# Kernel optimization log

Hardware: AMD Instinct MI355X
Metric: run time of the kernel (lower is better)

Reference implementation:

```python
import jax, jax.numpy as jnp
import numpy as np

B, T, NIN = 128, 256, 16
H1 = H2 = 512
NACT = 4
SLOPE = 25.0  # snntorch FastSigmoid default slope

@jax.custom_vjp
def spike(x):
    return (x > 0).astype(x.dtype)

def _spike_fwd(x):
    return (x > 0).astype(x.dtype), x

def _spike_bwd(x, g):
    # FastSigmoid surrogate: d/dx = 1 / (slope*|x| + 1)^2
    return (g / (SLOPE * jnp.abs(x) + 1.0) ** 2,)

spike.defvjp(_spike_fwd, _spike_bwd)

def setup_inputs() -> dict:
    key = jax.random.key(0)
    ks = jax.random.split(key, 12)
    def lin(k, fan_in, shape):
        lim = 1.0 / np.sqrt(fan_in)
        return jax.random.uniform(k, shape, jnp.float32, -lim, lim)
    return {
        "batch": jax.random.uniform(ks[0], (B, T, NIN), jnp.float32, 0.0, 2.5),
        "W1": lin(ks[1], NIN, (H1, NIN)), "b1": lin(ks[2], NIN, (H1,)),
        "beta1": jax.random.uniform(ks[3], (H1,), jnp.float32),
        "thr1": jax.random.uniform(ks[4], (H1,), jnp.float32),
        "W2": lin(ks[5], H1, (H2, H1)), "b2": lin(ks[6], H1, (H2,)),
        "beta2": jax.random.uniform(ks[7], (H2,), jnp.float32),
        "thr2": jax.random.uniform(ks[8], (H2,), jnp.float32),
        "Wa": lin(ks[9], H2, (NACT, H2)), "ba": lin(ks[10], H2, (NACT,)),
        "beta_act": jnp.float32(0.95),
        "inp_min": jnp.float32(0.0),
        "inp_max": jnp.float32(2.5),
    }

def _lif_subtract(cur, mem, beta, thr):
    # snntorch Leaky: reset from PRE-update membrane, detached; subtract reset
    reset = jax.lax.stop_gradient((mem - thr > 0).astype(mem.dtype))
    mem = jnp.clip(beta, 0.0, 1.0) * mem + cur - reset * thr
    return spike(mem - thr), mem

def reference(batch, W1, b1, beta1, thr1, W2, b2, beta2, thr2, Wa, ba, beta_act, inp_min, inp_max):
    Bb = batch.shape[0]
    x_seq = jnp.swapaxes(batch, 0, 1)  # [T, B, NIN]
    mem1 = jnp.zeros((Bb, W1.shape[0]), batch.dtype)
    mem2 = jnp.zeros((Bb, W2.shape[0]), batch.dtype)
    mem_a = jnp.zeros((Bb, Wa.shape[0]), batch.dtype)

    def step(carry, x):
        mem1, mem2, mem_a = carry
        x = (x - inp_min) / (inp_max - inp_min)
        spk1, mem1 = _lif_subtract(x @ W1.T + b1, mem1, beta1, thr1)
        spk2, mem2 = _lif_subtract(spk1 @ W2.T + b2, mem2, beta2, thr2)
        act = spk2 @ Wa.T + ba
        # action_lif: reset_mechanism='none', beta=0.95 learnable
        mem_a = jnp.clip(beta_act, 0.0, 1.0) * mem_a + act
        return (mem1, mem2, mem_a), mem_a.reshape(-1)  # torch: mem_act.reshape((1,-1))

    _, vals = jax.lax.scan(step, (mem1, mem2, mem_a), x_seq)
    # torch.stack(values, dim=1) of (1, B*NACT) tensors -> (1, T, B*NACT)
    return vals[None, :, :]
```

## Files before the change

### kernel.cpp

```cpp
#include <hip/hip_runtime.h>
#include <stdint.h>

typedef __attribute__((ext_vector_type(8))) short short8;
typedef __attribute__((ext_vector_type(4))) float f32x4;

#define T_STEPS 256
#define BATCH   128

#define LDS_BARRIER() asm volatile("s_waitcnt lgkmcnt(0)\n\ts_barrier" ::: "memory")

static __device__ inline unsigned short f2bf(float f) {
    unsigned int u = __float_as_uint(f);
    unsigned int r = u + 0x7FFFu + ((u >> 16) & 1u);
    return (unsigned short)(r >> 16);
}
static __device__ inline unsigned pack_hi16(unsigned a, unsigned b) {
    return (a >> 16) | (b & 0xFFFF0000u);
}

__global__ __launch_bounds__(256) void k_prep(
    const float* __restrict__ W2, const float* __restrict__ W1,
    const float* __restrict__ b1, const float* __restrict__ thr1,
    const float* __restrict__ imin_p, const float* __restrict__ imax_p,
    const float* __restrict__ batch,
    unsigned short* __restrict__ W2hi, unsigned short* __restrict__ W2lo,
    unsigned short* __restrict__ W1rows, float* __restrict__ b1s,
    unsigned short* __restrict__ Xf)
{
    int blk = blockIdx.x, tid = threadIdx.x;
    if (blk < 256) {
        int gid = blk * 256 + tid;
        f32x4 wv = *(const f32x4*)(W2 + (size_t)gid * 4);
        unsigned short hi[4], lo[4];
#pragma unroll
        for (int e = 0; e < 4; ++e) {
            float wf = wv[e];
            unsigned short h = f2bf(wf);
            float hf = __uint_as_float(((unsigned int)h) << 16);
            hi[e] = h;
            lo[e] = f2bf(wf - hf);
        }
        uint2 ph, pl;
        ph.x = (unsigned)hi[0] | ((unsigned)hi[1] << 16);
        ph.y = (unsigned)hi[2] | ((unsigned)hi[3] << 16);
        pl.x = (unsigned)lo[0] | ((unsigned)lo[1] << 16);
        pl.y = (unsigned)lo[2] | ((unsigned)lo[3] << 16);
        *(uint2*)(W2hi + (size_t)gid * 4) = ph;
        *(uint2*)(W2lo + (size_t)gid * 4) = pl;
    } else if (blk < 258) {
        int h = (blk - 256) * 256 + tid;
        float wsc = 1.0f / thr1[h];
        unsigned short row[64];
#pragma unroll
        for (int k = 0; k < 16; ++k) {
            float wv = W1[h * 16 + k] * wsc;
            unsigned a = __float_as_uint(wv) & 0xFFFF0000u;
            float r1 = wv - __uint_as_float(a);
            unsigned m = __float_as_uint(r1) & 0xFFFF0000u;
            float r2 = r1 - __uint_as_float(m);
            unsigned l = __float_as_uint(r2) & 0xFFFF0000u;
            row[k]      = (unsigned short)(a >> 16);
            row[16 + k] = (unsigned short)(m >> 16);
            row[32 + k] = (unsigned short)(l >> 16);
            row[48 + k] = 0;
        }
        b1s[h] = b1[h] * wsc;
        uint4* dst = (uint4*)(W1rows + (size_t)h * 64);
#pragma unroll
        for (int i = 0; i < 8; ++i) dst[i] = ((uint4*)row)[i];
    } else {
        int gid   = (blk - 258) * 256 + tid;
        int lane  = gid & 63;
        int btile = (gid >> 6) & 7;
        int t     = gid >> 9;
        int q     = lane >> 4, m15 = lane & 15;
        int b     = btile * 16 + m15;
        float imin = imin_p[0];
        float isc  = 1.0f / (imax_p[0] - imin);
        const float* xp = batch + ((size_t)b * T_STEPS + t) * 16 + (q & 1) * 8;
        unsigned uh[8], um[8], ul[8];
#pragma unroll
        for (int j = 0; j < 8; ++j) {
            float xv = (xp[j] - imin) * isc;
            unsigned a = __float_as_uint(xv) & 0xFFFF0000u;
            float r1 = xv - __uint_as_float(a);
            unsigned m = __float_as_uint(r1) & 0xFFFF0000u;
            float r2 = r1 - __uint_as_float(m);
            unsigned l = __float_as_uint(r2) & 0xFFFF0000u;
            uh[j] = a; um[j] = m; ul[j] = l;
        }
        uint4 B1, B2, XL;
        B1.x = pack_hi16(uh[0], uh[1]); B1.y = pack_hi16(uh[2], uh[3]);
        B1.z = pack_hi16(uh[4], uh[5]); B1.w = pack_hi16(uh[6], uh[7]);
        B2.x = pack_hi16(um[0], um[1]); B2.y = pack_hi16(um[2], um[3]);
        B2.z = pack_hi16(um[4], um[5]); B2.w = pack_hi16(um[6], um[7]);
        XL.x = pack_hi16(ul[0], ul[1]); XL.y = pack_hi16(ul[2], ul[3]);
        XL.z = pack_hi16(ul[4], ul[5]); XL.w = pack_hi16(ul[6], ul[7]);
        uint4 B3 = (q < 2) ? XL : B1;
        unsigned short* dst = Xf + (((size_t)t * 8 + btile) * 3) * 512 + lane * 8;
        *(uint4*)(dst +    0) = B1;
        *(uint4*)(dst +  512) = B2;
        *(uint4*)(dst + 1024) = B3;
    }
}

__global__ __launch_bounds__(1024, 4) void k_main(
    const unsigned short* __restrict__ Xf,
    const unsigned short* __restrict__ W2hi, const unsigned short* __restrict__ W2lo,
    const unsigned short* __restrict__ W1rows, const float* __restrict__ b1s,
    const float* __restrict__ beta1, const float* __restrict__ b2,
    const float* __restrict__ beta2, const float* __restrict__ thr2,
    unsigned short* __restrict__ spkbits)
{
    __shared__ unsigned short Aw[8192];
    __shared__ float Cbuf[2][4352];

    int tid  = threadIdx.x;
    int lane = tid & 63;
    int w    = tid >> 6;
    int q    = lane >> 4, m15 = lane & 15;
    int btile = blockIdx.x & 7;
    int slice = blockIdx.x >> 3;

    short8 A1[2], A2[2];
#pragma unroll
    for (int c = 0; c < 2; ++c) {
        const unsigned short* rp = W1rows + (size_t)(w * 32 + c * 16 + m15) * 64;
        A1[c] = *(const short8*)(rp + q * 8);
        A2[c] = *(const short8*)(rp + q * 8 + (q >> 1) * 16);
    }
    int jg = slice * 16 + m15;
    short8 bhi = *(const short8*)(W2hi + (size_t)jg * 512 + w * 32 + q * 8);
    short8 blo = *(const short8*)(W2lo + (size_t)jg * 512 + w * 32 + q * 8);

    f32x4 b14[2], bet1[2];
#pragma unroll
    for (int c = 0; c < 2; ++c) {
        int h0 = w * 32 + c * 16 + q * 4;
        b14[c] = *(const f32x4*)(b1s + h0);
        f32x4 bb = *(const f32x4*)(beta1 + h0);
#pragma unroll
        for (int r = 0; r < 4; ++r) bet1[c][r] = fminf(fmaxf(bb[r], 0.0f), 1.0f);
    }
    float m1[8], spk1f[8];
#pragma unroll
    for (int i = 0; i < 8; ++i) { m1[i] = 0.0f; spk1f[i] = 0.0f; }

    float beta2r = fminf(fmaxf(beta2[jg], 0.0f), 1.0f);
    float thr2r  = thr2[jg];
    float nthr2  = -thr2r;
    float b2r    = b2[jg];
    float m2 = 0.0f, spk2f = 0.0f;

    const unsigned short* xbase = Xf + ((size_t)btile * 3) * 512 + lane * 8;
    uint4 xc[3], xn[3];
#pragma unroll
    for (int f = 0; f < 3; ++f) xc[f] = *(const uint4*)(xbase + f * 512);

    unsigned short* myAw = Aw + w * 512;
    int wr0 = (0 * 2 + (q >> 1)) * 128 + (m15 ^ (q >> 1)) * 8 + (q & 1) * 4;
    int wr1 = (1 * 2 + (q >> 1)) * 128 + (m15 ^ (q >> 1)) * 8 + (q & 1) * 4;
    int rdo = (q * 16 + (m15 ^ (q & 1))) * 8;
    int p4  = (lane >> 4) * 4;

    auto body = [&](int ts, uint4* xcur, uint4* xnx) __attribute__((always_inline)) {
        int buf = ts & 1;
        int tn = (ts + 1 < T_STEPS) ? ts + 1 : ts;
        const unsigned short* xp = xbase + (size_t)tn * 12288;
#pragma unroll
        for (int f = 0; f < 3; ++f) xnx[f] = *(const uint4*)(xp + f * 512);

        union { uint4 u; short8 s; } Bf[3];
#pragma unroll
        for (int f = 0; f < 3; ++f) Bf[f].u = xcur[f];
        f32x4 D[2];
#pragma unroll
        for (int c = 0; c < 2; ++c) {
            D[c] = b14[c];
            D[c] = __builtin_amdgcn_mfma_f32_16x16x32_bf16(A1[c], Bf[0].s, D[c], 0, 0, 0);
            D[c] = __builtin_amdgcn_mfma_f32_16x16x32_bf16(A1[c], Bf[1].s, D[c], 0, 0, 0);
            D[c] = __builtin_amdgcn_mfma_f32_16x16x32_bf16(A2[c], Bf[2].s, D[c], 0, 0, 0);
        }
#pragma unroll
        for (int i = 0; i < 8; ++i) {
            int c = i >> 2, r = i & 3;
            float mv = fmaf(bet1[c][r], m1[i], D[c][r]);
            mv -= spk1f[i];
            bool sp = mv > 1.0f;
            m1[i] = mv;
            spk1f[i] = sp ? 1.0f : 0.0f;
        }
        {
            uint2 pk0, pk1;
            pk0.x = pack_hi16(__float_as_uint(spk1f[0]), __float_as_uint(spk1f[1]));
            pk0.y = pack_hi16(__float_as_uint(spk1f[2]), __float_as_uint(spk1f[3]));
            pk1.x = pack_hi16(__float_as_uint(spk1f[4]), __float_as_uint(spk1f[5]));
            pk1.y = pack_hi16(__float_as_uint(spk1f[6]), __float_as_uint(spk1f[7]));
            *(uint2*)(myAw + wr0) = pk0;
            *(uint2*)(myAw + wr1) = pk1;
        }
        union { uint4 u; short8 s; } af;
        af.u = *(uint4*)(myAw + rdo);
        f32x4 C2 = { 0.f, 0.f, 0.f, 0.f };
        C2 = __builtin_amdgcn_mfma_f32_16x16x32_bf16(af.s, bhi, C2, 0, 0, 0);
        C2 = __builtin_amdgcn_mfma_f32_16x16x32_bf16(af.s, blo, C2, 0, 0, 0);
#pragma unroll
        for (int r = 0; r < 4; ++r)
            Cbuf[buf][(q * 4 + r) * 272 + m15 * 17 + w] = C2[r];
        LDS_BARRIER();
        {
            float s0, s1, s2, s3;
            int base = w * 272 + m15 * 17 + p4;
            s0 = Cbuf[buf][base + 0];
            s1 = Cbuf[buf][base + 1];
            s2 = Cbuf[buf][base + 2];
            s3 = Cbuf[buf][base + 3];
            float s = (s0 + s1) + (s2 + s3);
            s += __shfl_xor(s, 16, 64);
            s += __shfl_xor(s, 32, 64);
            float cur2 = b2r + s;
            m2 = fmaf(beta2r, m2, cur2);
            m2 = fmaf(spk2f, nthr2, m2);
            bool sp2 = m2 > thr2r;
            spk2f = sp2 ? 1.0f : 0.0f;
            unsigned long long mask = __ballot(sp2);
            if (lane == 0) {
                spkbits[((size_t)ts * BATCH + btile * 16 + w) * 32 + slice] =
                    (unsigned short)(mask & 0xFFFFu);
            }
        }
    };

#pragma unroll 1
    for (int ts = 0; ts < T_STEPS; ts += 2) {
        body(ts, xc, xn);
        body(ts + 1, xn, xc);
    }
}

__global__ __launch_bounds__(256) void k_act(
    const unsigned short* __restrict__ spkbits,
    const float* __restrict__ Wa, const float* __restrict__ ba,
    const float* __restrict__ beta_act_p, float* __restrict__ out)
{
    __shared__ f32x4 waT[512];
    __shared__ f32x4 sc[256];
    int tid = threadIdx.x;
    int b   = blockIdx.x;

    for (int j = tid; j < 512; j += 256) {
        f32x4 v = { Wa[j], Wa[512 + j], Wa[1024 + j], Wa[1536 + j] };
        waT[j] = v;
    }
    float bact = fminf(fmaxf(beta_act_p[0], 0.0f), 1.0f);
    f32x4 acc = { ba[0], ba[1], ba[2], ba[3] };
    __syncthreads();

    const unsigned short* sp = spkbits + ((size_t)tid * BATCH + b) * 32;
    unsigned int wbuf[16];
#pragma unroll
    for (int r = 0; r < 4; ++r) {
        uint4 v = *(const uint4*)(sp + r * 8);
        wbuf[r*4+0] = v.x; wbuf[r*4+1] = v.y; wbuf[r*4+2] = v.z; wbuf[r*4+3] = v.w;
    }
    for (int s = 0; s < 32; ++s) {
        unsigned int wd = (wbuf[s >> 1] >> ((s & 1) * 16)) & 0xFFFFu;
#pragma unroll
        for (int i = 0; i < 16; ++i) {
            float sel = ((wd >> i) & 1u) ? 1.0f : 0.0f;
            f32x4 wv = waT[s * 16 + i];
            acc[0] = fmaf(sel, wv[0], acc[0]);
            acc[1] = fmaf(sel, wv[1], acc[1]);
            acc[2] = fmaf(sel, wv[2], acc[2]);
            acc[3] = fmaf(sel, wv[3], acc[3]);
        }
    }
    sc[tid] = acc;
    __syncthreads();
    float bd = bact;
    for (int d = 1; d < 256; d <<= 1) {
        f32x4 cv = sc[tid];
        f32x4 pv = { 0.f, 0.f, 0.f, 0.f };
        if (tid >= d) pv = sc[tid - d];
        __syncthreads();
        cv[0] = fmaf(bd, pv[0], cv[0]);
        cv[1] = fmaf(bd, pv[1], cv[1]);
        cv[2] = fmaf(bd, pv[2], cv[2]);
        cv[3] = fmaf(bd, pv[3], cv[3]);
        sc[tid] = cv;
        __syncthreads();
        bd *= bd;
    }
    f32x4 res = sc[tid];
    *(f32x4*)(out + (size_t)tid * 512 + b * 4) = res;
}

extern "C" void kernel_launch(void* const* d_in, const int* in_sizes, int n_in,
                              void* d_out, int out_size, void* d_ws, size_t ws_size,
                              hipStream_t stream)
{
    const float* batch    = (const float*)d_in[0];
    const float* W1       = (const float*)d_in[1];
    const float* b1       = (const float*)d_in[2];
    const float* beta1    = (const float*)d_in[3];
    const float* thr1     = (const float*)d_in[4];
    const float* W2       = (const float*)d_in[5];
    const float* b2       = (const float*)d_in[6];
    const float* beta2    = (const float*)d_in[7];
    const float* thr2     = (const float*)d_in[8];
    const float* Wa       = (const float*)d_in[9];
    const float* ba       = (const float*)d_in[10];
    const float* beta_act = (const float*)d_in[11];
    const float* inp_min  = (const float*)d_in[12];
    const float* inp_max  = (const float*)d_in[13];
    float* out            = (float*)d_out;

    char* ws = (char*)d_ws;
    unsigned short* W2hi    = (unsigned short*)ws;
    unsigned short* W2lo    = (unsigned short*)(ws + (512u << 10));
    unsigned short* W1rows  = (unsigned short*)(ws + (1u << 20));
    float*          b1s     = (float*)(ws + (1u << 20) + (64u << 10));
    unsigned short* Xf      = (unsigned short*)(ws + (2u << 20));
    unsigned short* spkbits = (unsigned short*)(ws + (8u << 20));

    hipLaunchKernelGGL(k_prep, dim3(770), dim3(256), 0, stream,
                       W2, W1, b1, thr1, inp_min, inp_max, batch,
                       W2hi, W2lo, W1rows, b1s, Xf);
    hipLaunchKernelGGL(k_main, dim3(256), dim3(1024), 0, stream,
                       Xf, W2hi, W2lo, W1rows, b1s, beta1, b2, beta2, thr2, spkbits);
    hipLaunchKernelGGL(k_act, dim3(128), dim3(256), 0, stream, spkbits, Wa, ba, beta_act, out);
}
```

Measured before the change: 313.4 us.

## Software-pipeline layer-1 compute with a two-stage LDS reduction of layer-2 partials

Restructures the main time loop so layer-1 MFMA work for step k+1 is issued before the cross-wave reduction of step k's layer-2 partial sums. The reduction is split into two LDS stages (Cbuf, then Sbuf) with a lane-contiguous layout, replacing the strided padded read and the shuffle-based reduction. Each wave now owns a subset of rows for the final LIF update. The aim is to hide the reduction latency behind the next step's compute, at the cost of an extra barrier per step and more LDS traffic.

```diff
diff --git a/kernel.cpp b/kernel.cpp
--- a/kernel.cpp
+++ b/kernel.cpp
@@ -113,7 +113,8 @@
     unsigned short* __restrict__ spkbits)
 {
     __shared__ unsigned short Aw[8192];
-    __shared__ float Cbuf[2][4352];
+    __shared__ float Cbuf[2][4096];
+    __shared__ float Sbuf[1024];
 
     int tid  = threadIdx.x;
     int lane = tid & 63;
@@ -121,6 +122,7 @@
     int q    = lane >> 4, m15 = lane & 15;
     int btile = blockIdx.x & 7;
     int slice = blockIdx.x >> 3;
+    int rr   = w & 3, gg = w >> 2;
 
     short8 A1[2], A2[2];
 #pragma unroll
@@ -153,19 +155,17 @@
     float m2 = 0.0f, spk2f = 0.0f;
 
     const unsigned short* xbase = Xf + ((size_t)btile * 3) * 512 + lane * 8;
-    uint4 xc[3], xn[3];
-#pragma unroll
-    for (int f = 0; f < 3; ++f) xc[f] = *(const uint4*)(xbase + f * 512);
+    uint4 xA[3], xB[3];
+#pragma unroll
+    for (int f = 0; f < 3; ++f) xA[f] = *(const uint4*)(xbase + f * 512);
 
     unsigned short* myAw = Aw + w * 512;
     int wr0 = (0 * 2 + (q >> 1)) * 128 + (m15 ^ (q >> 1)) * 8 + (q & 1) * 4;
     int wr1 = (1 * 2 + (q >> 1)) * 128 + (m15 ^ (q >> 1)) * 8 + (q & 1) * 4;
     int rdo = (q * 16 + (m15 ^ (q & 1))) * 8;
-    int p4  = (lane >> 4) * 4;
-
-    auto body = [&](int ts, uint4* xcur, uint4* xnx) __attribute__((always_inline)) {
-        int buf = ts & 1;
-        int tn = (ts + 1 < T_STEPS) ? ts + 1 : ts;
+
+    auto W = [&](int k, uint4* xcur, uint4* xnx) __attribute__((always_inline)) {
+        int tn = (k + 1 < T_STEPS) ? k + 1 : k;
         const unsigned short* xp = xbase + (size_t)tn * 12288;
 #pragma unroll
         for (int f = 0; f < 3; ++f) xnx[f] = *(const uint4*)(xp + f * 512);
@@ -204,37 +204,50 @@
         f32x4 C2 = { 0.f, 0.f, 0.f, 0.f };
         C2 = __builtin_amdgcn_mfma_f32_16x16x32_bf16(af.s, bhi, C2, 0, 0, 0);
         C2 = __builtin_amdgcn_mfma_f32_16x16x32_bf16(af.s, blo, C2, 0, 0, 0);
+        float* cb = Cbuf[k & 1];
 #pragma unroll
         for (int r = 0; r < 4; ++r)
-            Cbuf[buf][(q * 4 + r) * 272 + m15 * 17 + w] = C2[r];
+            cb[r * 1024 + w * 64 + lane] = C2[r];
+    };
+    auto S1 = [&](int i) __attribute__((always_inline)) {
+        const float* cb = Cbuf[i & 1];
+        float s0 = cb[rr * 1024 + (gg * 4 + 0) * 64 + lane];
+        float s1 = cb[rr * 1024 + (gg * 4 + 1) * 64 + lane];
+        float s2 = cb[rr * 1024 + (gg * 4 + 2) * 64 + lane];
+        float s3 = cb[rr * 1024 + (gg * 4 + 3) * 64 + lane];
+        Sbuf[(rr * 4 + gg) * 64 + lane] = (s0 + s1) + (s2 + s3);
+    };
+    auto S2 = [&](int i) __attribute__((always_inline)) {
+        float s0 = Sbuf[(rr * 4 + 0) * 64 + lane];
+        float s1 = Sbuf[(rr * 4 + 1) * 64 + lane];
+        float s2 = Sbuf[(rr * 4 + 2) * 64 + lane];
+        float s3 = Sbuf[(rr * 4 + 3) * 64 + lane];
+        float cur2 = b2r + ((s0 + s1) + (s2 + s3));
+        m2 = fmaf(beta2r, m2, cur2);
+        m2 = fmaf(spk2f, nthr2, m2);
+        bool sp2 = m2 > thr2r;
+        spk2f = sp2 ? 1.0f : 0.0f;
+        unsigned long long mask = __ballot(sp2);
+        if (w < 4 && m15 == 0) {
+            int p = lane >> 4;
+            spkbits[((size_t)i * BATCH + btile * 16 + p * 4 + w) * 32 + slice] =
+                (unsigned short)(mask >> (p * 16));
+        }
+    };
+
+    W(0, xA, xB);
+#pragma unroll 1
+    for (int i = 0; i < T_STEPS; i += 2) {
         LDS_BARRIER();
-        {
-            float s0, s1, s2, s3;
-            int base = w * 272 + m15 * 17 + p4;
-            s0 = Cbuf[buf][base + 0];
-            s1 = Cbuf[buf][base + 1];
-            s2 = Cbuf[buf][base + 2];
-            s3 = Cbuf[buf][base + 3];
-            float s = (s0 + s1) + (s2 + s3);
-            s += __shfl_xor(s, 16, 64);
-            s += __shfl_xor(s, 32, 64);
-            float cur2 = b2r + s;
-            m2 = fmaf(beta2r, m2, cur2);
-            m2 = fmaf(spk2f, nthr2, m2);
-            bool sp2 = m2 > thr2r;
-            spk2f = sp2 ? 1.0f : 0.0f;
-            unsigned long long mask = __ballot(sp2);
-            if (lane == 0) {
-                spkbits[((size_t)ts * BATCH + btile * 16 + w) * 32 + slice] =
-                    (unsigned short)(mask & 0xFFFFu);
-            }
-        }
-    };
-
-#pragma unroll 1
-    for (int ts = 0; ts < T_STEPS; ts += 2) {
-        body(ts, xc, xn);
-        body(ts + 1, xn, xc);
+        W(i + 1, xB, xA);
+        S1(i);
+        LDS_BARRIER();
+        S2(i);
+        LDS_BARRIER();
+        if (i + 2 < T_STEPS) W(i + 2, xA, xB);
+        S1(i + 1);
+        LDS_BARRIER();
+        S2(i + 1);
     }
 }
 
```

Result: slower. 332.5 us (+6.1%).

## Software-pipeline layer-2 reduction across timesteps with swizzled Cbuf layout

Applied to the files above, without the earlier changes.

Restructures the main time loop so each step's layer-2 reduction and spike emission run after the next step's layer-1 MFMA and LIF work. This lets the LDS reads overlap with compute, and the loop now needs only one barrier per step. The input prefetch distance is increased to two steps, and Cbuf switches from a padded stride-17 layout to an XOR-swizzled layout, which makes it smaller. The cost is extra register pressure from the deeper pipeline and a trickier prologue and epilogue, with a risk of off-by-one timing errors.

```diff
diff --git a/kernel.cpp b/kernel.cpp
--- a/kernel.cpp
+++ b/kernel.cpp
@@ -113,7 +113,7 @@
     unsigned short* __restrict__ spkbits)
 {
     __shared__ unsigned short Aw[8192];
-    __shared__ float Cbuf[2][4352];
+    __shared__ float Cbuf[2][4096];
 
     int tid  = threadIdx.x;
     int lane = tid & 63;
@@ -121,6 +121,7 @@
     int q    = lane >> 4, m15 = lane & 15;
     int btile = blockIdx.x & 7;
     int slice = blockIdx.x >> 3;
+    int rr = w & 3, qi = w >> 2;
 
     short8 A1[2], A2[2];
 #pragma unroll
@@ -153,34 +154,35 @@
     float m2 = 0.0f, spk2f = 0.0f;
 
     const unsigned short* xbase = Xf + ((size_t)btile * 3) * 512 + lane * 8;
-    uint4 xc[3], xn[3];
-#pragma unroll
-    for (int f = 0; f < 3; ++f) xc[f] = *(const uint4*)(xbase + f * 512);
-
-    unsigned short* myAw = Aw + w * 512;
-    int wr0 = (0 * 2 + (q >> 1)) * 128 + (m15 ^ (q >> 1)) * 8 + (q & 1) * 4;
-    int wr1 = (1 * 2 + (q >> 1)) * 128 + (m15 ^ (q >> 1)) * 8 + (q & 1) * 4;
+    const unsigned short* xpA = xbase + 2 * 12288;
+    const unsigned short* xpB = xbase + 3 * 12288;
+    uint4 xP[3], xQ[3];
+#pragma unroll
+    for (int f = 0; f < 3; ++f) xP[f] = *(const uint4*)(xbase + f * 512);
+#pragma unroll
+    for (int f = 0; f < 3; ++f) xQ[f] = *(const uint4*)(xbase + 12288 + f * 512);
+
+    unsigned short* awp = Aw + w * 512;
+    int wr0 = ((q >> 1)) * 128 + (m15 ^ (q >> 1)) * 8 + (q & 1) * 4;
+    int wr1 = wr0 + 256;
     int rdo = (q * 16 + (m15 ^ (q & 1))) * 8;
-    int p4  = (lane >> 4) * 4;
-
-    auto body = [&](int ts, uint4* xcur, uint4* xnx) __attribute__((always_inline)) {
-        int buf = ts & 1;
-        int tn = (ts + 1 < T_STEPS) ? ts + 1 : ts;
-        const unsigned short* xp = xbase + (size_t)tn * 12288;
-#pragma unroll
-        for (int f = 0; f < 3; ++f) xnx[f] = *(const uint4*)(xp + f * 512);
-
-        union { uint4 u; short8 s; } Bf[3];
-#pragma unroll
-        for (int f = 0; f < 3; ++f) Bf[f].u = xcur[f];
-        f32x4 D[2];
+    int sidx = w * 64 + (lane ^ (qi * 16));
+    int ridx = rr * 1024 + q * 256 + ((qi ^ q) * 16 + m15);
+
+    unsigned short* spkp = spkbits + ((size_t)btile * 16 + (qi * 4 + rr)) * 32 + slice;
+
+    auto gemm1 = [&](uint4* x, f32x4* D) __attribute__((always_inline)) {
+        union { uint4 u; short8 s; } B0, B1, B2;
+        B0.u = x[0]; B1.u = x[1]; B2.u = x[2];
 #pragma unroll
         for (int c = 0; c < 2; ++c) {
             D[c] = b14[c];
-            D[c] = __builtin_amdgcn_mfma_f32_16x16x32_bf16(A1[c], Bf[0].s, D[c], 0, 0, 0);
-            D[c] = __builtin_amdgcn_mfma_f32_16x16x32_bf16(A1[c], Bf[1].s, D[c], 0, 0, 0);
-            D[c] = __builtin_amdgcn_mfma_f32_16x16x32_bf16(A2[c], Bf[2].s, D[c], 0, 0, 0);
-        }
+            D[c] = __builtin_amdgcn_mfma_f32_16x16x32_bf16(A1[c], B0.s, D[c], 0, 0, 0);
+            D[c] = __builtin_amdgcn_mfma_f32_16x16x32_bf16(A1[c], B1.s, D[c], 0, 0, 0);
+            D[c] = __builtin_amdgcn_mfma_f32_16x16x32_bf16(A2[c], B2.s, D[c], 0, 0, 0);
+        }
+    };
+    auto lifpack = [&](f32x4* D) __attribute__((always_inline)) {
 #pragma unroll
         for (int i = 0; i < 8; ++i) {
             int c = i >> 2, r = i & 3;
@@ -190,51 +192,72 @@
             m1[i] = mv;
             spk1f[i] = sp ? 1.0f : 0.0f;
         }
-        {
-            uint2 pk0, pk1;
-            pk0.x = pack_hi16(__float_as_uint(spk1f[0]), __float_as_uint(spk1f[1]));
-            pk0.y = pack_hi16(__float_as_uint(spk1f[2]), __float_as_uint(spk1f[3]));
-            pk1.x = pack_hi16(__float_as_uint(spk1f[4]), __float_as_uint(spk1f[5]));
-            pk1.y = pack_hi16(__float_as_uint(spk1f[6]), __float_as_uint(spk1f[7]));
-            *(uint2*)(myAw + wr0) = pk0;
-            *(uint2*)(myAw + wr1) = pk1;
-        }
+        uint2 pk0, pk1;
+        pk0.x = pack_hi16(__float_as_uint(spk1f[0]), __float_as_uint(spk1f[1]));
+        pk0.y = pack_hi16(__float_as_uint(spk1f[2]), __float_as_uint(spk1f[3]));
+        pk1.x = pack_hi16(__float_as_uint(spk1f[4]), __float_as_uint(spk1f[5]));
+        pk1.y = pack_hi16(__float_as_uint(spk1f[6]), __float_as_uint(spk1f[7]));
+        *(uint2*)(awp + wr0) = pk0;
+        *(uint2*)(awp + wr1) = pk1;
+    };
+    auto rtail = [&](float s0, float s1, float s2, float s3) __attribute__((always_inline)) {
+        float s = (s0 + s1) + (s2 + s3);
+        s += __shfl_xor(s, 16, 64);
+        s += __shfl_xor(s, 32, 64);
+        m2 = fmaf(beta2r, m2, b2r + s);
+        m2 = fmaf(spk2f, nthr2, m2);
+        bool sp2 = m2 > thr2r;
+        spk2f = sp2 ? 1.0f : 0.0f;
+        unsigned long long mask = __ballot(sp2);
+        if (lane == 0) *spkp = (unsigned short)(mask & 0xFFFFu);
+        spkp += BATCH * 32;
+    };
+    auto g2sc = [&](float* cb) __attribute__((always_inline)) {
         union { uint4 u; short8 s; } af;
-        af.u = *(uint4*)(myAw + rdo);
+        af.u = *(uint4*)(awp + rdo);
         f32x4 C2 = { 0.f, 0.f, 0.f, 0.f };
         C2 = __builtin_amdgcn_mfma_f32_16x16x32_bf16(af.s, bhi, C2, 0, 0, 0);
         C2 = __builtin_amdgcn_mfma_f32_16x16x32_bf16(af.s, blo, C2, 0, 0, 0);
-#pragma unroll
-        for (int r = 0; r < 4; ++r)
-            Cbuf[buf][(q * 4 + r) * 272 + m15 * 17 + w] = C2[r];
+        cb[sidx]        = C2[0];
+        cb[sidx + 1024] = C2[1];
+        cb[sidx + 2048] = C2[2];
+        cb[sidx + 3072] = C2[3];
+    };
+
+    f32x4 D0[2], D1[2];
+    gemm1(xP, D0);
+
+#pragma unroll 1
+    for (int i = 0; i < T_STEPS; i += 2) {
+        {
+            const float* rb = Cbuf[1];
+            float s0 = rb[ridx], s1 = rb[ridx + 64], s2 = rb[ridx + 128], s3 = rb[ridx + 192];
+            lifpack(D0);
+#pragma unroll
+            for (int f = 0; f < 3; ++f) xP[f] = *(const uint4*)(xpA + f * 512);
+            xpA += 24576;
+            gemm1(xQ, D1);
+            if (i) rtail(s0, s1, s2, s3);
+            g2sc(Cbuf[0]);
+        }
         LDS_BARRIER();
         {
-            float s0, s1, s2, s3;
-            int base = w * 272 + m15 * 17 + p4;
-            s0 = Cbuf[buf][base + 0];
-            s1 = Cbuf[buf][base + 1];
-            s2 = Cbuf[buf][base + 2];
-            s3 = Cbuf[buf][base + 3];
-            float s = (s0 + s1) + (s2 + s3);
-            s += __shfl_xor(s, 16, 64);
-            s += __shfl_xor(s, 32, 64);
-            float cur2 = b2r + s;
-            m2 = fmaf(beta2r, m2, cur2);
-            m2 = fmaf(spk2f, nthr2, m2);
-            bool sp2 = m2 > thr2r;
-            spk2f = sp2 ? 1.0f : 0.0f;
-            unsigned long long mask = __ballot(sp2);
-            if (lane == 0) {
-                spkbits[((size_t)ts * BATCH + btile * 16 + w) * 32 + slice] =
-                    (unsigned short)(mask & 0xFFFFu);
-            }
-        }
-    };
-
-#pragma unroll 1
-    for (int ts = 0; ts < T_STEPS; ts += 2) {
-        body(ts, xc, xn);
-        body(ts + 1, xn, xc);
+            const float* rb = Cbuf[0];
+            float s0 = rb[ridx], s1 = rb[ridx + 64], s2 = rb[ridx + 128], s3 = rb[ridx + 192];
+            lifpack(D1);
+#pragma unroll
+            for (int f = 0; f < 3; ++f) xQ[f] = *(const uint4*)(xpB + f * 512);
+            xpB += 24576;
+            gemm1(xP, D0);
+            rtail(s0, s1, s2, s3);
+            g2sc(Cbuf[1]);
+        }
+        LDS_BARRIER();
+    }
+    {
+        const float* rb = Cbuf[1];
+        float s0 = rb[ridx], s1 = rb[ridx + 64], s2 = rb[ridx + 128], s3 = rb[ridx + 192];
+        rtail(s0, s1, s2, s3);
     }
 }
 
```

Result: no change. 308.7 us (-1.5%).
